# Optimization experiments

Measured on AMD Instinct MI355X. Metric: run time of the kernel, lower is better.

Reference implementation:

```python
import jax, jax.numpy as jnp
import numpy as np

B, S, D = 16, 4096, 64


def setup_inputs() -> dict:
    key = jax.random.key(0)
    kq, kk, kv = jax.random.split(key, 3)
    q = jax.random.normal(kq, (B, S, D), dtype=jnp.float32)
    k = jax.random.normal(kk, (B, S, D), dtype=jnp.float32)
    v = jax.random.normal(kv, (B, S, D), dtype=jnp.float32)
    inv_scale_factor = jnp.float32(1.0 / np.sqrt(D))  # source DIVIDES by this
    p = 0  # dropout prob (deterministic baseline -> identity)
    return {"q": q, "k": k, "v": v, "inv_scale_factor": inv_scale_factor, "p": p}


def reference(q, k, v, inv_scale_factor, p):
    # qk = q @ k^T ; scaled = qk / inv_scale_factor (faithful to source)
    scores = jnp.einsum("bsd,btd->bst", q, k) / inv_scale_factor  # [B,S,S]
    attn = jax.nn.softmax(scores, axis=-1)
    # dropout with p=0 is identity (eval-mode baseline)
    out = jnp.einsum("bst,btd->bsd", attn, v)  # [B,S,D]
    return out
```

## Files before the change

### kernel.cpp

```cpp
#include <hip/hip_runtime.h>
#include <hip/hip_bf16.h>

typedef float f32x4 __attribute__((ext_vector_type(4)));
typedef float f32x16 __attribute__((ext_vector_type(16)));
typedef _Float16 half8 __attribute__((ext_vector_type(8)));
typedef __bf16 bf16x8 __attribute__((ext_vector_type(8)));
typedef __bf16 bf16x4 __attribute__((ext_vector_type(4)));
typedef unsigned short ushort_t;

constexpr int Bb = 16, Ss = 4096, Dd = 64;
constexpr int KBLK = 32, QBLK = 128;
constexpr int NT = Ss / KBLK;
constexpr float kLOG2E = 1.44269504088896340736f;
constexpr float DEFER_THR = 10.0f;

constexpr int KP_BLOCKS = (Bb * Ss * Dd / 8) / 256;
constexpr int VT_BLOCKS = (Bb * Dd * (Ss / 32)) / 256;

#define GLOAD_LDS16(gp, lp)                                                              \
    __builtin_amdgcn_global_load_lds(                                                    \
        (const __attribute__((address_space(1))) void*)(gp),                             \
        (__attribute__((address_space(3))) void*)(lp), 16, 0, 0)

__global__ __launch_bounds__(256)
void prep_f16s(const float* __restrict__ K, const float* __restrict__ V,
               _Float16* __restrict__ Khi, _Float16* __restrict__ Klo,
               _Float16* __restrict__ Vt)
{
    const int bid = blockIdx.x;
    if (bid < KP_BLOCKS) {
        const size_t idx = ((size_t)bid * 256 + threadIdx.x) * 8;
        const float4 a = *reinterpret_cast<const float4*>(K + idx);
        const float4 c = *reinterpret_cast<const float4*>(K + idx + 4);
        float xs[8] = {a.x, a.y, a.z, a.w, c.x, c.y, c.z, c.w};
        half8 h8, l8;
#pragma unroll
        for (int i = 0; i < 8; ++i) {
            const _Float16 h = (_Float16)xs[i];
            h8[i] = h;
            l8[i] = (_Float16)(xs[i] - (float)h);
        }
        *reinterpret_cast<half8*>(Khi + idx) = h8;
        *reinterpret_cast<half8*>(Klo + idx) = l8;
    } else {
        const int t = (bid - KP_BLOCKS) * 256 + threadIdx.x;
        const int d = t & 63;
        const int s32 = (t >> 6) & (Ss / 32 - 1);
        const int b = t >> 13;
        const float* vp = V + ((size_t)b * Ss + (size_t)s32 * 32) * Dd + d;
        __align__(16) _Float16 ob[32];
#pragma unroll
        for (int j = 0; j < 32; ++j) ob[j] = (_Float16)vp[(size_t)j * Dd];
        _Float16* op = Vt + ((size_t)b * Dd + d) * Ss + (size_t)s32 * 32;
#pragma unroll
        for (int j8 = 0; j8 < 4; ++j8)
            *reinterpret_cast<half8*>(op + j8 * 8) = *reinterpret_cast<half8*>(ob + j8 * 8);
    }
}

union H8 { half8 h; unsigned int u[4]; };

__global__ __launch_bounds__(256, 2)
void attn_fwd_v10(const float* __restrict__ Q, const float* __restrict__ inv_scale,
                  const _Float16* __restrict__ Khi, const _Float16* __restrict__ Klo,
                  const _Float16* __restrict__ Vt, float* __restrict__ Out)
{
    __shared__ __align__(16) unsigned char smem[48 * 1024];

    const int tid = threadIdx.x;
    const int lane = tid & 63;
    const int w = tid >> 6;
    const int p = w & 1;
    const int qg = w >> 1;
    const int l31 = lane & 31;
    const int hi = lane >> 5;

    const int bid = (blockIdx.x & 7) * 64 + (blockIdx.x >> 3);
    const int b = bid >> 5;
    const int q0 = (bid & 31) * QBLK;

    const _Float16* KhB = Khi + (size_t)b * Ss * Dd;
    const _Float16* KlB = Klo + (size_t)b * Ss * Dd;
    const _Float16* VB = Vt + (size_t)b * Dd * Ss;

    const int kk = tid >> 3;
    const int ksrc = kk * Dd + (((tid & 7) ^ (kk & 7)) << 3);
    const int dd_ = tid >> 2;
    const size_t vsrc = (size_t)dd_ * Ss + (((tid & 3) ^ ((dd_ >> 1) & 3)) << 3);

#define STAGE(t)                                                                            \
    do {                                                                                    \
        GLOAD_LDS16(KhB + (size_t)(t) * (KBLK * Dd) + ksrc,                                 \
                    smem + ((t) & 3) * 4096 + tid * 16);                                    \
        GLOAD_LDS16(KlB + (size_t)(t) * (KBLK * Dd) + ksrc,                                 \
                    smem + 16384 + ((t) & 3) * 4096 + tid * 16);                            \
        GLOAD_LDS16(VB + (size_t)(t) * KBLK + vsrc,                                         \
                    smem + 32768 + ((t) & 3) * 4096 + tid * 16);                            \
    } while (0)

    STAGE(0);
    STAGE(1);

    int koff[4], voff[4];
#pragma unroll
    for (int ks = 0; ks < 4; ++ks)
        koff[ks] = l31 * 128 + ((((ks << 1) + hi) ^ (l31 & 7)) << 4);
#pragma unroll
    for (int i = 0; i < 4; ++i) {
        const int d = (i >> 1) * 32 + l31;
        voff[i] = d * 64 + (((((i & 1) << 1) + hi) ^ ((d >> 1) & 3)) << 4);
    }

    H8 qhi[2][4], qlo[2][4];
    {
        const float s2 = (1.0f / inv_scale[0]) * kLOG2E;
#pragma unroll
        for (int qs = 0; qs < 2; ++qs) {
            const float* qrow =
                Q + ((size_t)b * Ss + q0 + qg * 64 + qs * 32 + l31) * Dd;
#pragma unroll
            for (int ks = 0; ks < 4; ++ks) {
                const int d0 = ks * 16 + hi * 8;
                const float4 a = *reinterpret_cast<const float4*>(qrow + d0);
                const float4 cc = *reinterpret_cast<const float4*>(qrow + d0 + 4);
                float xs[8] = {a.x, a.y, a.z, a.w, cc.x, cc.y, cc.z, cc.w};
#pragma unroll
                for (int i = 0; i < 8; ++i) {
                    const float x = xs[i] * s2;
                    const _Float16 h = (_Float16)x;
                    qhi[qs][ks].h[i] = h;
                    qlo[qs][ks].h[i] = (_Float16)(x - (float)h);
                }
            }
        }
    }

    f32x16 O0, O1, O2, O3;
#pragma unroll
    for (int r = 0; r < 16; ++r) { O0[r] = 0.f; O1[r] = 0.f; O2[r] = 0.f; O3[r] = 0.f; }
    float m0 = -INFINITY, l0 = 0.f, m1 = -INFINITY, l1 = 0.f;

    auto xhalf = [&](unsigned int& a, unsigned int& cx) {
        const unsigned int y = hi ? a : cx;
        const unsigned int sy = __shfl_xor(y, 32);
        const unsigned int na = hi ? sy : a;
        const unsigned int nc = hi ? cx : sy;
        a = na; cx = nc;
    };

    __syncthreads();

    for (int it = 0; it < NT / 2; ++it) {
        const int t = 2 * it + p;
        const unsigned char* khbase = smem + (t & 3) * 4096;
        const unsigned char* klbase = smem + 16384 + (t & 3) * 4096;
        const unsigned char* vbase = smem + 32768 + (t & 3) * 4096;

        if (it < NT / 2 - 1) { STAGE(2 * it + 2); STAGE(2 * it + 3); }

        f32x16 S0, S1;
#pragma unroll
        for (int r = 0; r < 16; ++r) { S0[r] = 0.f; S1[r] = 0.f; }
        __builtin_amdgcn_s_setprio(1);
#pragma unroll
        for (int ks = 0; ks < 4; ++ks) {
            const half8 kh = *reinterpret_cast<const half8*>(khbase + koff[ks]);
            const half8 kl = *reinterpret_cast<const half8*>(klbase + koff[ks]);
            S0 = __builtin_amdgcn_mfma_f32_32x32x16_f16(kh, qhi[0][ks].h, S0, 0, 0, 0);
            S1 = __builtin_amdgcn_mfma_f32_32x32x16_f16(kh, qhi[1][ks].h, S1, 0, 0, 0);
            S0 = __builtin_amdgcn_mfma_f32_32x32x16_f16(kl, qhi[0][ks].h, S0, 0, 0, 0);
            S1 = __builtin_amdgcn_mfma_f32_32x32x16_f16(kl, qhi[1][ks].h, S1, 0, 0, 0);
            S0 = __builtin_amdgcn_mfma_f32_32x32x16_f16(kh, qlo[0][ks].h, S0, 0, 0, 0);
            S1 = __builtin_amdgcn_mfma_f32_32x32x16_f16(kh, qlo[1][ks].h, S1, 0, 0, 0);
        }
        __builtin_amdgcn_s_setprio(0);

        float t0 = S0[0], t1 = S1[0];
#pragma unroll
        for (int r = 1; r < 16; ++r) { t0 = fmaxf(t0, S0[r]); t1 = fmaxf(t1, S1[r]); }
        t0 = fmaxf(t0, __shfl_xor(t0, 32));
        t1 = fmaxf(t1, __shfl_xor(t1, 32));

        float fac0 = 1.0f, fac1 = 1.0f;
        if (__any(fmaxf(t0 - m0, t1 - m1) > DEFER_THR)) {
            const float mn0 = fmaxf(m0, t0);
            fac0 = __builtin_amdgcn_exp2f(m0 - mn0);
            m0 = mn0;
            const float mn1 = fmaxf(m1, t1);
            fac1 = __builtin_amdgcn_exp2f(m1 - mn1);
            m1 = mn1;
#pragma unroll
            for (int r = 0; r < 16; ++r) {
                O0[r] *= fac0; O1[r] *= fac0;
                O2[r] *= fac1; O3[r] *= fac1;
            }
        }

        float ts0 = 0.f, ts1 = 0.f;
#pragma unroll
        for (int r = 0; r < 16; ++r) {
            S0[r] = __builtin_amdgcn_exp2f(S0[r] - m0);
            ts0 += S0[r];
            S1[r] = __builtin_amdgcn_exp2f(S1[r] - m1);
            ts1 += S1[r];
        }
        ts0 += __shfl_xor(ts0, 32);
        ts1 += __shfl_xor(ts1, 32);
        l0 = l0 * fac0 + ts0;
        l1 = l1 * fac1 + ts1;

        unsigned int wa[8], wb[8];
#pragma unroll
        for (int j = 0; j < 8; ++j) {
            const auto ha = __builtin_amdgcn_cvt_pkrtz(S0[2 * j], S0[2 * j + 1]);
            wa[j] = __builtin_bit_cast(unsigned int, ha);
            const auto hb = __builtin_amdgcn_cvt_pkrtz(S1[2 * j], S1[2 * j + 1]);
            wb[j] = __builtin_bit_cast(unsigned int, hb);
        }
        xhalf(wa[0], wa[2]); xhalf(wa[1], wa[3]);
        xhalf(wa[4], wa[6]); xhalf(wa[5], wa[7]);
        xhalf(wb[0], wb[2]); xhalf(wb[1], wb[3]);
        xhalf(wb[4], wb[6]); xhalf(wb[5], wb[7]);

        H8 pa0, pa1, pb0, pb1;
        pa0.u[0] = wa[0]; pa0.u[1] = wa[1]; pa0.u[2] = wa[2]; pa0.u[3] = wa[3];
        pa1.u[0] = wa[4]; pa1.u[1] = wa[5]; pa1.u[2] = wa[6]; pa1.u[3] = wa[7];
        pb0.u[0] = wb[0]; pb0.u[1] = wb[1]; pb0.u[2] = wb[2]; pb0.u[3] = wb[3];
        pb1.u[0] = wb[4]; pb1.u[1] = wb[5]; pb1.u[2] = wb[6]; pb1.u[3] = wb[7];

        const half8 vf0 = *reinterpret_cast<const half8*>(vbase + voff[0]);
        const half8 vf1 = *reinterpret_cast<const half8*>(vbase + voff[1]);
        const half8 vf2 = *reinterpret_cast<const half8*>(vbase + voff[2]);
        const half8 vf3 = *reinterpret_cast<const half8*>(vbase + voff[3]);
        __builtin_amdgcn_s_setprio(1);
        O0 = __builtin_amdgcn_mfma_f32_32x32x16_f16(vf0, pa0.h, O0, 0, 0, 0);
        O2 = __builtin_amdgcn_mfma_f32_32x32x16_f16(vf0, pb0.h, O2, 0, 0, 0);
        O0 = __builtin_amdgcn_mfma_f32_32x32x16_f16(vf1, pa1.h, O0, 0, 0, 0);
        O2 = __builtin_amdgcn_mfma_f32_32x32x16_f16(vf1, pb1.h, O2, 0, 0, 0);
        O1 = __builtin_amdgcn_mfma_f32_32x32x16_f16(vf2, pa0.h, O1, 0, 0, 0);
        O3 = __builtin_amdgcn_mfma_f32_32x32x16_f16(vf2, pb0.h, O3, 0, 0, 0);
        O1 = __builtin_amdgcn_mfma_f32_32x32x16_f16(vf3, pa1.h, O1, 0, 0, 0);
        O3 = __builtin_amdgcn_mfma_f32_32x32x16_f16(vf3, pb1.h, O3, 0, 0, 0);
        __builtin_amdgcn_s_setprio(0);

        __syncthreads();
    }

    float* mO = (float*)smem;
    float* ml = (float*)(smem + 16384);

#define MERGE_ROUND(OA, OB, MV, LV, QS)                                                     \
    do {                                                                                    \
        if (p == 1) {                                                                       \
            _Pragma("unroll") for (int rr = 0; rr < 4; ++rr) {                              \
                f32x4 va, vb;                                                               \
                _Pragma("unroll") for (int j = 0; j < 4; ++j) {                             \
                    va[j] = OA[rr * 4 + j];                                                 \
                    vb[j] = OB[rr * 4 + j];                                                 \
                }                                                                           \
                *reinterpret_cast<f32x4*>(mO + (((qg * 2 + 0) * 4 + rr) << 8) + lane * 4) = \
                    va;                                                                     \
                *reinterpret_cast<f32x4*>(mO + (((qg * 2 + 1) * 4 + rr) << 8) + lane * 4) = \
                    vb;                                                                     \
            }                                                                               \
            if (hi == 0) {                                                                  \
                ml[qg * 64 + l31] = MV;                                                     \
                ml[qg * 64 + 32 + l31] = LV;                                                \
            }                                                                               \
        }                                                                                   \
        __syncthreads();                                                                    \
        if (p == 0) {                                                                       \
            const float m_o = ml[qg * 64 + l31];                                            \
            const float l_o = ml[qg * 64 + 32 + l31];                                       \
            const float mm = fmaxf(MV, m_o);                                                \
            float f0 = __builtin_amdgcn_exp2f(MV - mm);                                     \
            float f1 = __builtin_amdgcn_exp2f(m_o - mm);                                    \
            const float inv = 1.0f / (LV * f0 + l_o * f1);                                  \
            f0 *= inv; f1 *= inv;                                                           \
            float* orow = Out + ((size_t)b * Ss + q0 + qg * 64 + (QS) * 32 + l31) * Dd;     \
            _Pragma("unroll") for (int dblk = 0; dblk < 2; ++dblk) {                        \
                _Pragma("unroll") for (int rr = 0; rr < 4; ++rr) {                          \
                    const f32x4 ov = *reinterpret_cast<const f32x4*>(                       \
                        mO + (((qg * 2 + dblk) * 4 + rr) << 8) + lane * 4);                 \
                    f32x4 res;                                                              \
                    _Pragma("unroll") for (int j = 0; j < 4; ++j) {                         \
                        const float mine =                                                  \
                            (dblk == 0) ? OA[rr * 4 + j] : OB[rr * 4 + j];                  \
                        res[j] = mine * f0 + ov[j] * f1;                                    \
                    }                                                                       \
                    *reinterpret_cast<f32x4*>(orow + dblk * 32 + rr * 8 + hi * 4) = res;    \
                }                                                                           \
            }                                                                               \
        }                                                                                   \
        __syncthreads();                                                                    \
    } while (0)

    MERGE_ROUND(O0, O1, m0, l0, 0);
    MERGE_ROUND(O2, O3, m1, l1, 1);
#undef MERGE_ROUND
#undef STAGE
}

__global__ __launch_bounds__(256)
void attn_fwd_fallback(const float* __restrict__ Q, const float* __restrict__ K,
                       const float* __restrict__ V, const float* __restrict__ inv_scale,
                       float* __restrict__ Out)
{
    __shared__ __align__(16) ushort_t sKhi[KBLK * Dd];
    __shared__ __align__(16) ushort_t sKlo[KBLK * Dd];
    __shared__ __align__(16) ushort_t sVt[Dd * KBLK];
    __shared__ __align__(16) ushort_t sP[4][16 * KBLK];

    const int tid = threadIdx.x;
    const int lane = tid & 63;
    const int w = tid >> 6;
    const int q15 = lane & 15;
    const int g = lane >> 4;
    const int b = blockIdx.x >> 6;
    const int q0 = (blockIdx.x & 63) * 64;
    const float scale = 1.0f / inv_scale[0];

    const float* qptr = Q + (((size_t)b * Ss) + q0 + w * 16 + q15) * Dd;
    bf16x8 qhi[2], qlo[2];
#pragma unroll
    for (int ds = 0; ds < 2; ++ds) {
        const float4 f0 = *reinterpret_cast<const float4*>(qptr + ds * 32 + g * 8);
        const float4 f1 = *reinterpret_cast<const float4*>(qptr + ds * 32 + g * 8 + 4);
        float xs[8] = {f0.x, f0.y, f0.z, f0.w, f1.x, f1.y, f1.z, f1.w};
#pragma unroll
        for (int i = 0; i < 8; ++i) {
            __bf16 h = (__bf16)xs[i];
            qhi[ds][i] = h;
            qlo[ds][i] = (__bf16)(xs[i] - (float)h);
        }
    }
    const int krs = tid >> 3;
    const int kc8 = (tid & 7) * 8;
    const int kidx = krs * Dd + (kc8 ^ ((krs & 7) << 3));
    const float* kbase = K + ((size_t)b * Ss) * Dd;
    const int vd = tid & 63;
    const int vk8 = (tid >> 6) * 8;
    const int vidx = vd * KBLK + (vk8 ^ ((vd & 3) << 3));
    const float* vbase = V + ((size_t)b * Ss) * Dd;

    f32x4 Oacc[4];
#pragma unroll
    for (int dt = 0; dt < 4; ++dt)
#pragma unroll
        for (int r = 0; r < 4; ++r) Oacc[dt][r] = 0.f;
    float m_run = -INFINITY, l_run = 0.f;

    for (int k0 = 0; k0 < Ss; k0 += KBLK) {
        {
            const float* p0 = kbase + (size_t)(k0 + krs) * Dd + kc8;
            const float4 a = *reinterpret_cast<const float4*>(p0);
            const float4 c = *reinterpret_cast<const float4*>(p0 + 4);
            float xs[8] = {a.x, a.y, a.z, a.w, c.x, c.y, c.z, c.w};
            bf16x8 h8, l8;
#pragma unroll
            for (int i = 0; i < 8; ++i) {
                __bf16 h = (__bf16)xs[i];
                h8[i] = h;
                l8[i] = (__bf16)(xs[i] - (float)h);
            }
            *reinterpret_cast<bf16x8*>(&sKhi[kidx]) = h8;
            *reinterpret_cast<bf16x8*>(&sKlo[kidx]) = l8;
        }
        {
            bf16x8 v8;
#pragma unroll
            for (int j = 0; j < 8; ++j) v8[j] = (__bf16)vbase[(size_t)(k0 + vk8 + j) * Dd + vd];
            *reinterpret_cast<bf16x8*>(&sVt[vidx]) = v8;
        }
        __syncthreads();

        float z[2][4];
#pragma unroll
        for (int t = 0; t < 2; ++t) {
            const int krow = t * 16 + q15;
            f32x4 acc;
            acc[0] = acc[1] = acc[2] = acc[3] = 0.f;
#pragma unroll
            for (int ds = 0; ds < 2; ++ds) {
                const int ci = (ds * 32 + g * 8) ^ ((krow & 7) << 3);
                const bf16x8 kh = *reinterpret_cast<const bf16x8*>(&sKhi[krow * Dd + ci]);
                const bf16x8 kl = *reinterpret_cast<const bf16x8*>(&sKlo[krow * Dd + ci]);
                acc = __builtin_amdgcn_mfma_f32_16x16x32_bf16(kh, qhi[ds], acc, 0, 0, 0);
                acc = __builtin_amdgcn_mfma_f32_16x16x32_bf16(kl, qhi[ds], acc, 0, 0, 0);
                acc = __builtin_amdgcn_mfma_f32_16x16x32_bf16(kh, qlo[ds], acc, 0, 0, 0);
            }
#pragma unroll
            for (int r = 0; r < 4; ++r) z[t][r] = acc[r] * scale;
        }

        float tmax = z[0][0];
#pragma unroll
        for (int t = 0; t < 2; ++t)
#pragma unroll
            for (int r = 0; r < 4; ++r) tmax = fmaxf(tmax, z[t][r]);
        tmax = fmaxf(tmax, __shfl_xor(tmax, 16));
        tmax = fmaxf(tmax, __shfl_xor(tmax, 32));
        const float m_new = fmaxf(m_run, tmax);

        float pz[2][4];
        float tsum = 0.f;
#pragma unroll
        for (int t = 0; t < 2; ++t)
#pragma unroll
            for (int r = 0; r < 4; ++r) {
                const float e = __builtin_amdgcn_exp2f((z[t][r] - m_new) * kLOG2E);
                pz[t][r] = e;
                tsum += e;
            }
        tsum += __shfl_xor(tsum, 16);
        tsum += __shfl_xor(tsum, 32);
        const float fac = __builtin_amdgcn_exp2f((m_run - m_new) * kLOG2E);
        l_run = l_run * fac + tsum;
        m_run = m_new;

#pragma unroll
        for (int t = 0; t < 2; ++t) {
            bf16x4 pb;
#pragma unroll
            for (int r = 0; r < 4; ++r) pb[r] = (__bf16)pz[t][r];
            const int pidx = q15 * KBLK + ((t * 16 + g * 4) ^ ((q15 & 3) << 3));
            *reinterpret_cast<bf16x4*>(&sP[w][pidx]) = pb;
        }
        {
            const float fr0 = __shfl(fac, g * 4 + 0);
            const float fr1 = __shfl(fac, g * 4 + 1);
            const float fr2 = __shfl(fac, g * 4 + 2);
            const float fr3 = __shfl(fac, g * 4 + 3);
#pragma unroll
            for (int dt = 0; dt < 4; ++dt) {
                Oacc[dt][0] *= fr0; Oacc[dt][1] *= fr1;
                Oacc[dt][2] *= fr2; Oacc[dt][3] *= fr3;
            }
        }
        const int paidx = q15 * KBLK + ((g * 8) ^ ((q15 & 3) << 3));
        const bf16x8 pa = *reinterpret_cast<const bf16x8*>(&sP[w][paidx]);
#pragma unroll
        for (int dt = 0; dt < 4; ++dt) {
            const int dd = dt * 16 + q15;
            const bf16x8 vf =
                *reinterpret_cast<const bf16x8*>(&sVt[dd * KBLK + ((g * 8) ^ ((dd & 3) << 3))]);
            Oacc[dt] = __builtin_amdgcn_mfma_f32_16x16x32_bf16(pa, vf, Oacc[dt], 0, 0, 0);
        }
        __syncthreads();
    }

    const float invl = 1.0f / l_run;
    float il[4];
#pragma unroll
    for (int r = 0; r < 4; ++r) il[r] = __shfl(invl, g * 4 + r);
    float* obase = Out + (((size_t)b * Ss) + q0 + w * 16) * Dd;
#pragma unroll
    for (int dt = 0; dt < 4; ++dt)
#pragma unroll
        for (int r = 0; r < 4; ++r)
            obase[(size_t)(g * 4 + r) * Dd + dt * 16 + q15] = Oacc[dt][r] * il[r];
}

extern "C" void kernel_launch(void* const* d_in, const int* in_sizes, int n_in,
                              void* d_out, int out_size, void* d_ws, size_t ws_size,
                              hipStream_t stream)
{
    const float* q = (const float*)d_in[0];
    const float* k = (const float*)d_in[1];
    const float* v = (const float*)d_in[2];
    const float* inv_scale = (const float*)d_in[3];
    float* out = (float*)d_out;
    (void)in_sizes; (void)n_in; (void)out_size;

    const size_t NKV = (size_t)Bb * Ss * Dd;
    const size_t need = NKV * 3 * sizeof(_Float16);

    if (ws_size >= need) {
        _Float16* Khi = (_Float16*)d_ws;
        _Float16* Klo = Khi + NKV;
        _Float16* Vt = Klo + NKV;
        hipLaunchKernelGGL(prep_f16s, dim3(KP_BLOCKS + VT_BLOCKS), dim3(256), 0, stream,
                           k, v, Khi, Klo, Vt);
        hipLaunchKernelGGL(attn_fwd_v10, dim3(Bb * (Ss / QBLK)), dim3(256), 0, stream,
                           q, inv_scale, Khi, Klo, Vt, out);
    } else {
        hipLaunchKernelGGL(attn_fwd_fallback, dim3(Bb * 64), dim3(256), 0, stream,
                           q, k, v, inv_scale, out);
    }
}
```

Before: 175.5 us.

## Double query block to 256 and split KV four ways in 1024-thread blocks

Raises the query block to 256 rows and launches 1024-thread blocks. Each of four wave groups handles every fourth KV tile from an 8-slot LDS ring, and the four partial softmax states are merged at the end. Each staged K/V tile now serves twice as many queries, which cuts global/L2 traffic and issue overhead, and one block fills each CU. In exchange the per-wave register budget is tighter under the new launch bounds, which risks spills, LDS use roughly doubles, and the final merge reads three partial results per output.

```diff
diff --git a/kernel.cpp b/kernel.cpp
--- a/kernel.cpp
+++ b/kernel.cpp
@@ -9,7 +9,7 @@
 typedef unsigned short ushort_t;
 
 constexpr int Bb = 16, Ss = 4096, Dd = 64;
-constexpr int KBLK = 32, QBLK = 128;
+constexpr int KBLK = 32, QBLK = 256;
 constexpr int NT = Ss / KBLK;
 constexpr float kLOG2E = 1.44269504088896340736f;
 constexpr float DEFER_THR = 10.0f;
@@ -60,46 +60,47 @@
 
 union H8 { half8 h; unsigned int u[4]; };
 
-__global__ __launch_bounds__(256, 2)
-void attn_fwd_v10(const float* __restrict__ Q, const float* __restrict__ inv_scale,
+__global__ __launch_bounds__(1024, 4)
+void attn_fwd_v11(const float* __restrict__ Q, const float* __restrict__ inv_scale,
                   const _Float16* __restrict__ Khi, const _Float16* __restrict__ Klo,
                   const _Float16* __restrict__ Vt, float* __restrict__ Out)
 {
-    __shared__ __align__(16) unsigned char smem[48 * 1024];
+    __shared__ __align__(16) unsigned char smem[99 * 1024];
 
     const int tid = threadIdx.x;
     const int lane = tid & 63;
     const int w = tid >> 6;
-    const int p = w & 1;
-    const int qg = w >> 1;
+    const int p = w & 3;
+    const int qg = w >> 2;
     const int l31 = lane & 31;
     const int hi = lane >> 5;
 
-    const int bid = (blockIdx.x & 7) * 64 + (blockIdx.x >> 3);
-    const int b = bid >> 5;
-    const int q0 = (bid & 31) * QBLK;
+    const int bid = (blockIdx.x & 7) * 32 + (blockIdx.x >> 3);
+    const int b = bid >> 4;
+    const int q0 = (bid & 15) * QBLK;
 
     const _Float16* KhB = Khi + (size_t)b * Ss * Dd;
     const _Float16* KlB = Klo + (size_t)b * Ss * Dd;
     const _Float16* VB = Vt + (size_t)b * Dd * Ss;
 
-    const int kk = tid >> 3;
-    const int ksrc = kk * Dd + (((tid & 7) ^ (kk & 7)) << 3);
-    const int dd_ = tid >> 2;
-    const size_t vsrc = (size_t)dd_ * Ss + (((tid & 3) ^ ((dd_ >> 1) & 3)) << 3);
-
-#define STAGE(t)                                                                            \
+    const int c = tid & 255;
+    const int j4 = tid >> 8;
+    const int kk = c >> 3;
+    const int ksrc = kk * Dd + (((c & 7) ^ (kk & 7)) << 3);
+    const int dd_ = c >> 2;
+    const size_t vsrc = (size_t)dd_ * Ss + (((c & 3) ^ ((dd_ >> 1) & 3)) << 3);
+
+#define STAGE4(g)                                                                           \
     do {                                                                                    \
-        GLOAD_LDS16(KhB + (size_t)(t) * (KBLK * Dd) + ksrc,                                 \
-                    smem + ((t) & 3) * 4096 + tid * 16);                                    \
-        GLOAD_LDS16(KlB + (size_t)(t) * (KBLK * Dd) + ksrc,                                 \
-                    smem + 16384 + ((t) & 3) * 4096 + tid * 16);                            \
-        GLOAD_LDS16(VB + (size_t)(t) * KBLK + vsrc,                                         \
-                    smem + 32768 + ((t) & 3) * 4096 + tid * 16);                            \
+        const int _t = 4 * (g) + j4;                                                        \
+        const int _sl = _t & 7;                                                             \
+        GLOAD_LDS16(KhB + (size_t)_t * (KBLK * Dd) + ksrc, smem + _sl * 4096 + c * 16);     \
+        GLOAD_LDS16(KlB + (size_t)_t * (KBLK * Dd) + ksrc,                                  \
+                    smem + 32768 + _sl * 4096 + c * 16);                                    \
+        GLOAD_LDS16(VB + (size_t)_t * KBLK + vsrc, smem + 65536 + _sl * 4096 + c * 16);     \
     } while (0)
 
-    STAGE(0);
-    STAGE(1);
+    STAGE4(0);
 
     int koff[4], voff[4];
 #pragma unroll
@@ -116,8 +117,7 @@
         const float s2 = (1.0f / inv_scale[0]) * kLOG2E;
 #pragma unroll
         for (int qs = 0; qs < 2; ++qs) {
-            const float* qrow =
-                Q + ((size_t)b * Ss + q0 + qg * 64 + qs * 32 + l31) * Dd;
+            const float* qrow = Q + ((size_t)b * Ss + q0 + qg * 64 + qs * 32 + l31) * Dd;
 #pragma unroll
             for (int ks = 0; ks < 4; ++ks) {
                 const int d0 = ks * 16 + hi * 8;
@@ -150,13 +150,13 @@
 
     __syncthreads();
 
-    for (int it = 0; it < NT / 2; ++it) {
-        const int t = 2 * it + p;
-        const unsigned char* khbase = smem + (t & 3) * 4096;
-        const unsigned char* klbase = smem + 16384 + (t & 3) * 4096;
-        const unsigned char* vbase = smem + 32768 + (t & 3) * 4096;
-
-        if (it < NT / 2 - 1) { STAGE(2 * it + 2); STAGE(2 * it + 3); }
+    for (int it = 0; it < NT / 4; ++it) {
+        const int t = 4 * it + p;
+        const unsigned char* khbase = smem + (t & 7) * 4096;
+        const unsigned char* klbase = smem + 32768 + (t & 7) * 4096;
+        const unsigned char* vbase = smem + 65536 + (t & 7) * 4096;
+
+        if (it < NT / 4 - 1) STAGE4(it + 1);
 
         f32x16 S0, S1;
 #pragma unroll
@@ -247,46 +247,58 @@
     }
 
     float* mO = (float*)smem;
-    float* ml = (float*)(smem + 16384);
+    float* ml = (float*)(smem + 96 * 1024);
 
 #define MERGE_ROUND(OA, OB, MV, LV, QS)                                                     \
     do {                                                                                    \
-        if (p == 1) {                                                                       \
+        if (p != 0) {                                                                       \
+            const int pr = p - 1;                                                           \
             _Pragma("unroll") for (int rr = 0; rr < 4; ++rr) {                              \
                 f32x4 va, vb;                                                               \
                 _Pragma("unroll") for (int j = 0; j < 4; ++j) {                             \
                     va[j] = OA[rr * 4 + j];                                                 \
                     vb[j] = OB[rr * 4 + j];                                                 \
                 }                                                                           \
-                *reinterpret_cast<f32x4*>(mO + (((qg * 2 + 0) * 4 + rr) << 8) + lane * 4) = \
-                    va;                                                                     \
-                *reinterpret_cast<f32x4*>(mO + (((qg * 2 + 1) * 4 + rr) << 8) + lane * 4) = \
-                    vb;                                                                     \
+                *reinterpret_cast<f32x4*>(                                                  \
+                    mO + pr * 8192 + (((qg * 2 + 0) * 4 + rr) << 8) + lane * 4) = va;       \
+                *reinterpret_cast<f32x4*>(                                                  \
+                    mO + pr * 8192 + (((qg * 2 + 1) * 4 + rr) << 8) + lane * 4) = vb;       \
             }                                                                               \
             if (hi == 0) {                                                                  \
-                ml[qg * 64 + l31] = MV;                                                     \
-                ml[qg * 64 + 32 + l31] = LV;                                                \
+                ml[pr * 256 + qg * 64 + l31] = MV;                                          \
+                ml[pr * 256 + qg * 64 + 32 + l31] = LV;                                     \
             }                                                                               \
         }                                                                                   \
         __syncthreads();                                                                    \
         if (p == 0) {                                                                       \
-            const float m_o = ml[qg * 64 + l31];                                            \
-            const float l_o = ml[qg * 64 + 32 + l31];                                       \
-            const float mm = fmaxf(MV, m_o);                                                \
+            float ms[3], ls[3];                                                             \
+            float mm = MV;                                                                  \
+            _Pragma("unroll") for (int i = 0; i < 3; ++i) {                                 \
+                ms[i] = ml[i * 256 + qg * 64 + l31];                                        \
+                ls[i] = ml[i * 256 + qg * 64 + 32 + l31];                                   \
+                mm = fmaxf(mm, ms[i]);                                                      \
+            }                                                                               \
             float f0 = __builtin_amdgcn_exp2f(MV - mm);                                     \
-            float f1 = __builtin_amdgcn_exp2f(m_o - mm);                                    \
-            const float inv = 1.0f / (LV * f0 + l_o * f1);                                  \
-            f0 *= inv; f1 *= inv;                                                           \
+            float fi[3];                                                                    \
+            float denom = LV * f0;                                                          \
+            _Pragma("unroll") for (int i = 0; i < 3; ++i) {                                 \
+                fi[i] = __builtin_amdgcn_exp2f(ms[i] - mm);                                 \
+                denom += ls[i] * fi[i];                                                     \
+            }                                                                               \
+            const float inv = 1.0f / denom;                                                 \
+            f0 *= inv;                                                                      \
+            fi[0] *= inv; fi[1] *= inv; fi[2] *= inv;                                       \
             float* orow = Out + ((size_t)b * Ss + q0 + qg * 64 + (QS) * 32 + l31) * Dd;     \
             _Pragma("unroll") for (int dblk = 0; dblk < 2; ++dblk) {                        \
                 _Pragma("unroll") for (int rr = 0; rr < 4; ++rr) {                          \
-                    const f32x4 ov = *reinterpret_cast<const f32x4*>(                       \
-                        mO + (((qg * 2 + dblk) * 4 + rr) << 8) + lane * 4);                 \
                     f32x4 res;                                                              \
-                    _Pragma("unroll") for (int j = 0; j < 4; ++j) {                         \
-                        const float mine =                                                  \
-                            (dblk == 0) ? OA[rr * 4 + j] : OB[rr * 4 + j];                  \
-                        res[j] = mine * f0 + ov[j] * f1;                                    \
+                    _Pragma("unroll") for (int j = 0; j < 4; ++j)                           \
+                        res[j] = ((dblk == 0) ? OA[rr * 4 + j] : OB[rr * 4 + j]) * f0;      \
+                    _Pragma("unroll") for (int i = 0; i < 3; ++i) {                         \
+                        const f32x4 ov = *reinterpret_cast<const f32x4*>(                   \
+                            mO + i * 8192 + (((qg * 2 + dblk) * 4 + rr) << 8) + lane * 4);  \
+                        _Pragma("unroll") for (int j = 0; j < 4; ++j)                       \
+                            res[j] += ov[j] * fi[i];                                        \
                     }                                                                       \
                     *reinterpret_cast<f32x4*>(orow + dblk * 32 + rr * 8 + hi * 4) = res;    \
                 }                                                                           \
@@ -298,7 +310,7 @@
     MERGE_ROUND(O0, O1, m0, l0, 0);
     MERGE_ROUND(O2, O3, m1, l1, 1);
 #undef MERGE_ROUND
-#undef STAGE
+#undef STAGE4
 }
 
 __global__ __launch_bounds__(256)
@@ -481,7 +493,7 @@
         _Float16* Vt = Klo + NKV;
         hipLaunchKernelGGL(prep_f16s, dim3(KP_BLOCKS + VT_BLOCKS), dim3(256), 0, stream,
                            k, v, Khi, Klo, Vt);
-        hipLaunchKernelGGL(attn_fwd_v10, dim3(Bb * (Ss / QBLK)), dim3(256), 0, stream,
+        hipLaunchKernelGGL(attn_fwd_v11, dim3(Bb * (Ss / QBLK)), dim3(1024), 0, stream,
                            q, inv_scale, Khi, Klo, Vt, out);
     } else {
         hipLaunchKernelGGL(attn_fwd_fallback, dim3(Bb * 64), dim3(256), 0, stream,
```

Measured after the change: 413.3 us. 2.35x slower.
